# Kernel tuning notes

Measured on AMD Instinct MI355X. Metric: run time of the kernel, lower is better.

## Reference

```python
import jax, jax.numpy as jnp
import numpy as np

COV_EMB = 32
N_HEAD = 2
FACTOR_TCL = 2   # TemporalConvolutionalLayer factor (default 2)
FACTOR_MLP = 1   # MLP factor passed from MultiAttention init
EPS = 1e-5


def _conv1d_causal(x, w, b):
    # x: [N, C, T], w: [O, C, 3]; torch pads 2 both sides then slices [..., :-2],
    # equivalent to left-pad 2 only -> output length T.
    y = jax.lax.conv_general_dilated(x, w, window_strides=(1,), padding=[(2, 0)],
                                     dimension_numbers=('NCH', 'OIH', 'NCH'))
    return y + b[None, :, None]


def _tcl(x, w_conv, b_conv, w_proj, b_proj):
    # TemporalConvolutionalLayer: x [..., T, C] -> [..., T, C]
    shp = x.shape
    T, C = shp[-2], shp[-1]
    x2 = x.reshape(-1, T, C).transpose(0, 2, 1)              # [N, C, T]
    h = jax.nn.gelu(_conv1d_causal(x2, w_conv, b_conv), approximate=False)
    h = h.transpose(0, 2, 1)                                  # [N, T, 2C]
    out = h @ w_proj.T + b_proj                               # [N, T, C]
    return out.reshape(*shp[:-1], C)


def _layernorm(x, w):
    mu = jnp.mean(x, axis=-1, keepdims=True)
    var = jnp.var(x, axis=-1, keepdims=True)
    return (x - mu) * jax.lax.rsqrt(var + EPS) * w


def setup_inputs() -> dict:
    key = jax.random.key(0)
    ks = jax.random.split(key, 20)
    C = COV_EMB
    C2 = FACTOR_TCL * C
    s = 0.02
    inp = {
        'causal_decoder': jax.random.normal(ks[0], (8, 4, 1024, C), jnp.float32),
        'past_kv': jax.random.normal(ks[1], (8, 1024, C), jnp.float32),
    }
    def tcl_params(i):
        return (jax.random.normal(ks[i], (C2, C, 3), jnp.float32) * s,
                jnp.zeros((C2,), jnp.float32),
                jax.random.normal(ks[i + 1], (C, C2), jnp.float32) * s,
                jnp.zeros((C,), jnp.float32))
    inp['wq_conv'], inp['bq_conv'], inp['wq_proj'], inp['bq_proj'] = tcl_params(2)
    inp['wk_conv'], inp['bk_conv'], inp['wk_proj'], inp['bk_proj'] = tcl_params(4)
    inp['wv_conv'], inp['bv_conv'], inp['wv_proj'], inp['bv_proj'] = tcl_params(6)
    inp['w_cproj'] = jax.random.normal(ks[8], (C, C), jnp.float32) * s   # bias=False
    inp['ln_w'] = jnp.ones((C,), jnp.float32)                            # bias=False
    inp['w_fc'] = jax.random.normal(ks[9], (FACTOR_MLP * C, C), jnp.float32) * s   # bias=False
    inp['w_mlp_proj'] = jax.random.normal(ks[10], (C, FACTOR_MLP * C), jnp.float32) * s
    return inp


def reference(causal_decoder, past_kv,
              wq_conv, bq_conv, wq_proj, bq_proj,
              wk_conv, bk_conv, wk_proj, bk_proj,
              wv_conv, bv_conv, wv_proj, bv_proj,
              w_cproj, ln_w, w_fc, w_mlp_proj):
    B, F, T, C = causal_decoder.shape
    nh, hd = N_HEAD, C // N_HEAD

    q = _tcl(causal_decoder, wq_conv, bq_conv, wq_proj, bq_proj)   # [B,F,T,C]
    k = _tcl(past_kv, wk_conv, bk_conv, wk_proj, bk_proj)          # [B,S,C]
    v = _tcl(past_kv, wv_conv, bv_conv, wv_proj, bv_proj)          # [B,S,C]

    S = k.shape[1]
    q = q.reshape(B, F, T, nh, hd).transpose(0, 1, 3, 2, 4)        # [B,F,h,T,d]
    k = k.reshape(B, S, nh, hd).transpose(0, 2, 1, 3)              # [B,h,S,d]
    v = v.reshape(B, S, nh, hd).transpose(0, 2, 1, 3)              # [B,h,S,d]

    scale = 1.0 / jnp.sqrt(jnp.asarray(hd, q.dtype))
    scores = jnp.einsum('bfhtd,bhsd->bfhts', q, k) * scale          # [B,F,h,T,S]
    attn = jax.nn.softmax(scores, axis=-1)
    y = jnp.einsum('bfhts,bhsd->bfhtd', attn, v)                    # [B,F,h,T,d]
    y = y.transpose(0, 1, 3, 2, 4).reshape(B, F, T, C)

    out = causal_decoder + y @ w_cproj.T                            # resid_dropout = id (p=0)
    h = _layernorm(out, ln_w)
    mlp = jax.nn.gelu(h @ w_fc.T, approximate=False) @ w_mlp_proj.T
    out = out + mlp
    return out
```

## Files before the change

kernel.cpp:

```cpp
#include <hip/hip_runtime.h>
#include <hip/hip_bf16.h>

#define T_LEN 1024

typedef __attribute__((ext_vector_type(8))) short short8;
typedef __attribute__((ext_vector_type(4))) short short4v;
typedef __attribute__((ext_vector_type(4))) float float4v;
typedef __attribute__((ext_vector_type(2))) unsigned uint2v;
typedef __attribute__((ext_vector_type(4))) unsigned uint4v;

__device__ __forceinline__ float gelu_exact(float x) {
    return 0.5f * x * (1.0f + erff(x * 0.70710678118654752440f));
}
__device__ __forceinline__ unsigned short f2bf(float f) {
    unsigned u = __float_as_uint(f);
    u += 0x7fffu + ((u >> 16) & 1u);
    return (unsigned short)(u >> 16);
}
__device__ __forceinline__ unsigned pk2bf(float a, float b) {
    __hip_bfloat162 h = __float22bfloat162_rn(make_float2(a, b));
    unsigned u;
    __builtin_memcpy(&u, &h, 4);
    return u;
}

__device__ __forceinline__ short8 xpose_p(float4v t0, float4v t1) {
    unsigned u0 = pk2bf(t0.x, t0.y);
    unsigned u1 = pk2bf(t0.z, t0.w);
    unsigned u2 = pk2bf(t1.x, t1.y);
    unsigned u3 = pk2bf(t1.z, t1.w);
    uint2v r0 = __builtin_amdgcn_permlane32_swap(u0, u2, false, false);
    uint2v r1 = __builtin_amdgcn_permlane32_swap(u1, u3, false, false);
    uint2v r2 = __builtin_amdgcn_permlane16_swap(r0.x, r0.y, false, false);
    uint2v r3 = __builtin_amdgcn_permlane16_swap(r1.x, r1.y, false, false);
    uint4v p = { r2.x, r3.x, r2.y, r3.y };
    short8 f;
    __builtin_memcpy(&f, &p, 16);
    return f;
}

__global__ __launch_bounds__(256) void kv_tcl(
    const float* __restrict__ pkv,
    const float* __restrict__ wkc, const float* __restrict__ bkc,
    const float* __restrict__ wkp, const float* __restrict__ bkp,
    const float* __restrict__ wvc, const float* __restrict__ bvc,
    const float* __restrict__ wvp, const float* __restrict__ bvp,
    unsigned short* __restrict__ kbf, unsigned short* __restrict__ vtbf)
{
    __shared__ __align__(16) unsigned short Abuf[32 * 96];
    __shared__ __align__(16) unsigned short WbT[64 * 96];
    __shared__ __align__(16) unsigned short Hb[32 * 72];
    __shared__ __align__(16) unsigned short WpB[32 * 72];

    const int tid = threadIdx.x;
    const int gb = blockIdx.x;

    const float *wc, *bc, *wp, *bp;
    unsigned short* outb;
    int mode;
    if (gb < 256) { wc = wkc; bc = bkc; wp = wkp; bp = bkp; outb = kbf;  mode = 0; }
    else          { wc = wvc; bc = bvc; wp = wvp; bp = bvp; outb = vtbf; mode = 1; }
    const int n  = gb & 7;
    const int t0 = ((gb >> 3) & 31) * 32;

#pragma unroll
    for (int it = 0; it < 3; ++it) {
        int s = (tid + it * 256) >> 3;
        int sub = tid & 7;
        int t = s / 3, tap = s - t * 3;
        int tau = t0 + t - 2 + tap;
        float4 xv = make_float4(0.f, 0.f, 0.f, 0.f);
        if (tau >= 0) xv = *(const float4*)&pkv[((size_t)n * T_LEN + tau) * 32 + sub * 4];
        short4v pk = { (short)f2bf(xv.x), (short)f2bf(xv.y),
                       (short)f2bf(xv.z), (short)f2bf(xv.w) };
        *(short4v*)&Abuf[t * 96 + tap * 32 + sub * 4] = pk;
    }
#pragma unroll
    for (int it = 0; it < 6; ++it) {
        int i4 = tid + it * 256;
        int idx = i4 * 4;
        int o = idx / 96, r = idx - o * 96;
        float4 w4 = *(const float4*)&wc[idx];
        float we[4] = { w4.x, w4.y, w4.z, w4.w };
#pragma unroll
        for (int e = 0; e < 4; ++e) {
            int re = r + e, c = re / 3, tap = re - c * 3;
            WbT[o * 96 + tap * 32 + c] = f2bf(we[e]);
        }
    }
#pragma unroll
    for (int it = 0; it < 2; ++it) {
        int i4 = tid + it * 256;
        int idx = i4 * 4;
        int c = idx >> 6, o = idx & 63;
        float4 w4 = *(const float4*)&wp[idx];
        short4v pk = { (short)f2bf(w4.x), (short)f2bf(w4.y),
                       (short)f2bf(w4.z), (short)f2bf(w4.w) };
        *(short4v*)&WpB[c * 72 + o] = pk;
    }

    const int w = tid >> 6;
    const int ln = tid & 63;
    const int sn = ln & 15;
    const int quad = ln >> 4;

    const float bcv = bc[w * 16 + sn];
    const int tmw = w & 1, cnw = w >> 1;
    const float bpv = bp[cnw * 16 + sn];

    __syncthreads();

    short8 b0 = *(const short8*)&WbT[(w * 16 + sn) * 96 + 0  + quad * 8];
    short8 b1 = *(const short8*)&WbT[(w * 16 + sn) * 96 + 32 + quad * 8];
    short8 b2 = *(const short8*)&WbT[(w * 16 + sn) * 96 + 64 + quad * 8];
    float4v zero = { 0.f, 0.f, 0.f, 0.f };
    float4v acc[2] = { zero, zero };
#pragma unroll
    for (int tm = 0; tm < 2; ++tm) {
        const unsigned short* ar = &Abuf[(tm * 16 + sn) * 96 + quad * 8];
        short8 a0 = *(const short8*)(ar + 0);
        short8 a1 = *(const short8*)(ar + 32);
        short8 a2 = *(const short8*)(ar + 64);
        acc[tm] = __builtin_amdgcn_mfma_f32_16x16x32_bf16(a0, b0, acc[tm], 0, 0, 0);
        acc[tm] = __builtin_amdgcn_mfma_f32_16x16x32_bf16(a1, b1, acc[tm], 0, 0, 0);
        acc[tm] = __builtin_amdgcn_mfma_f32_16x16x32_bf16(a2, b2, acc[tm], 0, 0, 0);
    }
#pragma unroll
    for (int tm = 0; tm < 2; ++tm) {
        float ge[4];
        ge[0] = gelu_exact(acc[tm].x + bcv);
        ge[1] = gelu_exact(acc[tm].y + bcv);
        ge[2] = gelu_exact(acc[tm].z + bcv);
        ge[3] = gelu_exact(acc[tm].w + bcv);
#pragma unroll
        for (int i = 0; i < 4; ++i)
            Hb[(tm * 16 + quad * 4 + i) * 72 + w * 16 + sn] = f2bf(ge[i]);
    }

    __syncthreads();

    const unsigned short* hr = &Hb[(tmw * 16 + sn) * 72 + quad * 8];
    short8 pa0 = *(const short8*)(hr + 0);
    short8 pa1 = *(const short8*)(hr + 32);
    short8 pb0 = *(const short8*)&WpB[(cnw * 16 + sn) * 72 + quad * 8];
    short8 pb1 = *(const short8*)&WpB[(cnw * 16 + sn) * 72 + 32 + quad * 8];
    float4v pacc = zero;
    pacc = __builtin_amdgcn_mfma_f32_16x16x32_bf16(pa0, pb0, pacc, 0, 0, 0);
    pacc = __builtin_amdgcn_mfma_f32_16x16x32_bf16(pa1, pb1, pacc, 0, 0, 0);

    float v[4] = { pacc.x + bpv, pacc.y + bpv, pacc.z + bpv, pacc.w + bpv };
#pragma unroll
    for (int i = 0; i < 4; ++i) {
        int t = tmw * 16 + quad * 4 + i;
        int c = cnw * 16 + sn;
        if (mode == 0) {
            outb[((size_t)n * T_LEN + t0 + t) * 32 + c] = f2bf(v[i]);
        } else {
            outb[((size_t)(n * 2 + cnw) * 16 + sn) * T_LEN + t0 + t] = f2bf(v[i]);
        }
    }
}

__global__ __launch_bounds__(512) void fused_qae(
    const float* __restrict__ cd,
    const float* __restrict__ wqc, const float* __restrict__ bqc,
    const float* __restrict__ wqp, const float* __restrict__ bqp,
    const unsigned short* __restrict__ kbf,
    const unsigned short* __restrict__ vtbf,
    const float* __restrict__ wcp, const float* __restrict__ lnw,
    const float* __restrict__ wfc, const float* __restrict__ wmp,
    float* __restrict__ out)
{
    __shared__ __align__(16) char smem[43520];
    unsigned short* Abuf = (unsigned short*)(smem);
    unsigned short* WbT  = (unsigned short*)(smem + 12288);
    unsigned short* Hb   = (unsigned short*)(smem + 24576);
    unsigned short* WpB  = (unsigned short*)(smem + 33792);
    unsigned short* qs   = (unsigned short*)(smem + 38400);

    const int tid = threadIdx.x;
    const int bid = blockIdx.x;
    const int b  = bid & 7;
    const int f_ = (bid >> 3) & 3;
    const int bf = b * 4 + f_;
    const int tt = bid >> 5;
    const int t0 = tt * 64;
    const float SC = 0.36067376022224085f;

#pragma unroll
    for (int it = 0; it < 3; ++it) {
        int idx = tid + it * 512;
        int s = idx >> 3;
        int sub = idx & 7;
        int t = s / 3, tap = s - t * 3;
        int tau = t0 + t - 2 + tap;
        float4 xv = make_float4(0.f, 0.f, 0.f, 0.f);
        if (tau >= 0) xv = *(const float4*)&cd[((size_t)bf * T_LEN + tau) * 32 + sub * 4];
        short4v pk = { (short)f2bf(xv.x), (short)f2bf(xv.y),
                       (short)f2bf(xv.z), (short)f2bf(xv.w) };
        *(short4v*)&Abuf[t * 96 + tap * 32 + sub * 4] = pk;
    }
#pragma unroll
    for (int it = 0; it < 3; ++it) {
        int i4 = tid + it * 512;
        int idx = i4 * 4;
        int o = idx / 96, r = idx - o * 96;
        float4 w4 = *(const float4*)&wqc[idx];
        float we[4] = { w4.x, w4.y, w4.z, w4.w };
#pragma unroll
        for (int e = 0; e < 4; ++e) {
            int re = r + e, c = re / 3, tap = re - c * 3;
            WbT[o * 96 + tap * 32 + c] = f2bf(we[e]);
        }
    }
    {
        int idx = tid * 4;
        int c = idx >> 6, o = idx & 63;
        float4 w4 = *(const float4*)&wqp[idx];
        short4v pk = { (short)f2bf(w4.x), (short)f2bf(w4.y),
                       (short)f2bf(w4.z), (short)f2bf(w4.w) };
        *(short4v*)&WpB[c * 72 + o] = pk;
    }

    const int w = tid >> 6;
    const int ln = tid & 63;
    const int sn = ln & 15;
    const int quad = ln >> 4;
    const float4v zero = { 0.f, 0.f, 0.f, 0.f };

    __syncthreads();

    {
        const int tm = w & 3;
        const int on0 = w >> 2, on1 = on0 + 2;
        const unsigned short* ar = &Abuf[(tm * 16 + sn) * 96 + quad * 8];
        short8 a0 = *(const short8*)(ar + 0);
        short8 a1 = *(const short8*)(ar + 32);
        short8 a2 = *(const short8*)(ar + 64);
        const unsigned short* br0 = &WbT[(on0 * 16 + sn) * 96 + quad * 8];
        const unsigned short* br1 = &WbT[(on1 * 16 + sn) * 96 + quad * 8];
        float4v c0 = zero, c1 = zero;
        c0 = __builtin_amdgcn_mfma_f32_16x16x32_bf16(a0, *(const short8*)(br0 + 0),  c0, 0, 0, 0);
        c0 = __builtin_amdgcn_mfma_f32_16x16x32_bf16(a1, *(const short8*)(br0 + 32), c0, 0, 0, 0);
        c0 = __builtin_amdgcn_mfma_f32_16x16x32_bf16(a2, *(const short8*)(br0 + 64), c0, 0, 0, 0);
        c1 = __builtin_amdgcn_mfma_f32_16x16x32_bf16(a0, *(const short8*)(br1 + 0),  c1, 0, 0, 0);
        c1 = __builtin_amdgcn_mfma_f32_16x16x32_bf16(a1, *(const short8*)(br1 + 32), c1, 0, 0, 0);
        c1 = __builtin_amdgcn_mfma_f32_16x16x32_bf16(a2, *(const short8*)(br1 + 64), c1, 0, 0, 0);
        const float bc0 = bqc[on0 * 16 + sn], bc1 = bqc[on1 * 16 + sn];
        float g0[4] = { gelu_exact(c0.x + bc0), gelu_exact(c0.y + bc0),
                        gelu_exact(c0.z + bc0), gelu_exact(c0.w + bc0) };
        float g1[4] = { gelu_exact(c1.x + bc1), gelu_exact(c1.y + bc1),
                        gelu_exact(c1.z + bc1), gelu_exact(c1.w + bc1) };
#pragma unroll
        for (int i = 0; i < 4; ++i) {
            Hb[(tm * 16 + quad * 4 + i) * 72 + on0 * 16 + sn] = f2bf(g0[i]);
            Hb[(tm * 16 + quad * 4 + i) * 72 + on1 * 16 + sn] = f2bf(g1[i]);
        }
    }
    __syncthreads();

    {
        const int tm = w & 3, cn = w >> 2;
        const unsigned short* hr = &Hb[(tm * 16 + sn) * 72 + quad * 8];
        short8 pa0 = *(const short8*)(hr + 0);
        short8 pa1 = *(const short8*)(hr + 32);
        const unsigned short* wr_ = &WpB[(cn * 16 + sn) * 72 + quad * 8];
        short8 pb0 = *(const short8*)(wr_ + 0);
        short8 pb1 = *(const short8*)(wr_ + 32);
        float4v pacc = zero;
        pacc = __builtin_amdgcn_mfma_f32_16x16x32_bf16(pa0, pb0, pacc, 0, 0, 0);
        pacc = __builtin_amdgcn_mfma_f32_16x16x32_bf16(pa1, pb1, pacc, 0, 0, 0);
        const float bpv = bqp[cn * 16 + sn];
        float v[4] = { (pacc.x + bpv) * SC, (pacc.y + bpv) * SC,
                       (pacc.z + bpv) * SC, (pacc.w + bpv) * SC };
#pragma unroll
        for (int i = 0; i < 4; ++i)
            qs[(tm * 16 + quad * 4 + i) * 40 + cn * 16 + sn] = f2bf(v[i]);
    }

    {
        float* swc = (float*)(smem + 0);
        float* swf = (float*)(smem + 4608);
        float* swm = (float*)(smem + 9216);
        float* sln = (float*)(smem + 13824);
        for (int i = tid; i < 1024; i += 512) {
            int r = i >> 5, cc = i & 31;
            swc[r * 36 + cc] = wcp[i];
            swf[r * 36 + cc] = wfc[i];
            swm[r * 36 + cc] = wmp[i];
        }
        if (tid < 32) sln[tid] = lnw[tid];
    }
    __syncthreads();

    const int h = w & 1, rt = w >> 1;
    short8 aq = {0, 0, 0, 0, 0, 0, 0, 0};
    if (quad < 2)
        aq = *(const short8*)&qs[(rt * 16 + sn) * 40 + h * 16 + quad * 8];

    const unsigned short* kb = kbf + (size_t)b * T_LEN * 32 + h * 16 + quad * 8;
    const unsigned short* vb = vtbf + ((size_t)(b * 2 + h) * 16 + sn) * T_LEN + quad * 8;

    const short8 ones = { 16256, 16256, 16256, 16256,
                          16256, 16256, 16256, 16256 };
    float4v yacc = zero;
    float4v lacc = zero;

#pragma unroll 2
    for (int s0 = 0; s0 < 1024; s0 += 64) {
        short8 ka0 = {0,0,0,0,0,0,0,0}, ka1 = ka0, kc0 = ka0, kc1 = ka0;
        if (quad < 2) {
            ka0 = *(const short8*)(kb + (size_t)(s0 + sn) * 32);
            ka1 = *(const short8*)(kb + (size_t)(s0 + 16 + sn) * 32);
            kc0 = *(const short8*)(kb + (size_t)(s0 + 32 + sn) * 32);
            kc1 = *(const short8*)(kb + (size_t)(s0 + 48 + sn) * 32);
        }
        short8 bvA = *(const short8*)(vb + s0);
        short8 bvB = *(const short8*)(vb + s0 + 32);

        float4v cA0 = __builtin_amdgcn_mfma_f32_16x16x32_bf16(ka0, aq, zero, 0, 0, 0);
        float4v cA1 = __builtin_amdgcn_mfma_f32_16x16x32_bf16(ka1, aq, zero, 0, 0, 0);
        float4v cB0 = __builtin_amdgcn_mfma_f32_16x16x32_bf16(kc0, aq, zero, 0, 0, 0);
        float4v cB1 = __builtin_amdgcn_mfma_f32_16x16x32_bf16(kc1, aq, zero, 0, 0, 0);

        float4v eA0, eA1, eB0, eB1;
        eA0.x = exp2f(cA0.x); eA0.y = exp2f(cA0.y); eA0.z = exp2f(cA0.z); eA0.w = exp2f(cA0.w);
        eA1.x = exp2f(cA1.x); eA1.y = exp2f(cA1.y); eA1.z = exp2f(cA1.z); eA1.w = exp2f(cA1.w);
        eB0.x = exp2f(cB0.x); eB0.y = exp2f(cB0.y); eB0.z = exp2f(cB0.z); eB0.w = exp2f(cB0.w);
        eB1.x = exp2f(cB1.x); eB1.y = exp2f(cB1.y); eB1.z = exp2f(cB1.z); eB1.w = exp2f(cB1.w);

        short8 apA = xpose_p(eA0, eA1);
        short8 apB = xpose_p(eB0, eB1);

        yacc = __builtin_amdgcn_mfma_f32_16x16x32_bf16(bvA, apA, yacc, 0, 0, 0);
        yacc = __builtin_amdgcn_mfma_f32_16x16x32_bf16(bvB, apB, yacc, 0, 0, 0);
        lacc = __builtin_amdgcn_mfma_f32_16x16x32_bf16(ones, apA, lacc, 0, 0, 0);
        lacc = __builtin_amdgcn_mfma_f32_16x16x32_bf16(ones, apB, lacc, 0, 0, 0);
    }

    float* sy = (float*)(smem + 24576);
    {
        const float linv = 1.0f / lacc.x;
        float4v yn = { yacc.x * linv, yacc.y * linv,
                       yacc.z * linv, yacc.w * linv };
        *(float4v*)&sy[(rt * 16 + sn) * 32 + h * 16 + quad * 4] = yn;
    }
    __syncthreads();

    float* swc = (float*)(smem + 0);
    float* swf = (float*)(smem + 4608);
    float* swm = (float*)(smem + 9216);
    float* sln = (float*)(smem + 13824);
    float* shn = (float*)(smem + 13952);
    float* sgv = (float*)(smem + 16256);

    const int rl = tid >> 5, c = tid & 31;
    const float lnwc = sln[c];
#pragma unroll 1
    for (int p = 0; p < 4; ++p) {
        int r = p * 16 + rl;
        size_t row = (size_t)bf * T_LEN + t0 + r;
        float x1 = cd[row * 32 + c];
#pragma unroll
        for (int j4 = 0; j4 < 8; ++j4) {
            float4 yv = *(const float4*)&sy[r * 32 + j4 * 4];
            const float* wv = &swc[c * 36 + j4 * 4];
            x1 += wv[0] * yv.x + wv[1] * yv.y + wv[2] * yv.z + wv[3] * yv.w;
        }
        float s1 = x1, s2 = x1 * x1;
#pragma unroll
        for (int off = 16; off; off >>= 1) {
            s1 += __shfl_xor(s1, off);
            s2 += __shfl_xor(s2, off);
        }
        float mu = s1 * (1.0f / 32.0f);
        float var = s2 * (1.0f / 32.0f) - mu * mu;
        float hn = (x1 - mu) * rsqrtf(var + 1e-5f) * lnwc;
        shn[rl * 36 + c] = hn;
        float ga = 0.f;
#pragma unroll
        for (int j4 = 0; j4 < 8; ++j4) {
            float4 hv = *(const float4*)&shn[rl * 36 + j4 * 4];
            const float* wv = &swf[c * 36 + j4 * 4];
            ga += wv[0] * hv.x + wv[1] * hv.y + wv[2] * hv.z + wv[3] * hv.w;
        }
        float gv = gelu_exact(ga);
        sgv[rl * 36 + c] = gv;
        float oa = x1;
#pragma unroll
        for (int j4 = 0; j4 < 8; ++j4) {
            float4 gvv = *(const float4*)&sgv[rl * 36 + j4 * 4];
            const float* wv = &swm[c * 36 + j4 * 4];
            oa += wv[0] * gvv.x + wv[1] * gvv.y + wv[2] * gvv.z + wv[3] * gvv.w;
        }
        out[row * 32 + c] = oa;
    }
}

extern "C" void kernel_launch(void* const* d_in, const int* in_sizes, int n_in,
                              void* d_out, int out_size, void* d_ws, size_t ws_size,
                              hipStream_t stream) {
    const float* cd  = (const float*)d_in[0];
    const float* pkv = (const float*)d_in[1];
    const float* wqc = (const float*)d_in[2];
    const float* bqc = (const float*)d_in[3];
    const float* wqp = (const float*)d_in[4];
    const float* bqp = (const float*)d_in[5];
    const float* wkc = (const float*)d_in[6];
    const float* bkc = (const float*)d_in[7];
    const float* wkp = (const float*)d_in[8];
    const float* bkp = (const float*)d_in[9];
    const float* wvc = (const float*)d_in[10];
    const float* bvc = (const float*)d_in[11];
    const float* wvp = (const float*)d_in[12];
    const float* bvp = (const float*)d_in[13];
    const float* wcp = (const float*)d_in[14];
    const float* lnw = (const float*)d_in[15];
    const float* wfc = (const float*)d_in[16];
    const float* wmp = (const float*)d_in[17];

    unsigned short* kbf  = (unsigned short*)d_ws;
    unsigned short* vtbf = kbf + (size_t)8 * 1024 * 32;

    kv_tcl<<<512, 256, 0, stream>>>(pkv, wkc, bkc, wkp, bkp,
                                    wvc, bvc, wvp, bvp, kbf, vtbf);
    fused_qae<<<512, 512, 0, stream>>>(cd, wqc, bqc, wqp, bqp, kbf, vtbf,
                                       wcp, lnw, wfc, wmp, (float*)d_out);
}
```

Before: 133.9 us.

## Move Q TCL into the K/V TCL kernel and store scaled Q to global

The Q temporal-conv projection is taken out of the fused attention kernel and computed by the first kernel, which now launches 1536 blocks covering K, V and Q. Q is written to workspace as pre-scaled bf16, and the attention/epilogue kernel reads it from global memory. The attention kernel gets smaller LDS use and less prologue work, which may raise occupancy and shorten its critical path. In exchange there is an extra global round trip for Q and a larger first kernel.

```diff
diff --git a/kernel.cpp b/kernel.cpp
--- a/kernel.cpp
+++ b/kernel.cpp
@@ -39,13 +39,16 @@
     return f;
 }
 
-__global__ __launch_bounds__(256) void kv_tcl(
-    const float* __restrict__ pkv,
+__global__ __launch_bounds__(256) void tcl_all(
+    const float* __restrict__ cd, const float* __restrict__ pkv,
+    const float* __restrict__ wqc, const float* __restrict__ bqc,
+    const float* __restrict__ wqp, const float* __restrict__ bqp,
     const float* __restrict__ wkc, const float* __restrict__ bkc,
     const float* __restrict__ wkp, const float* __restrict__ bkp,
     const float* __restrict__ wvc, const float* __restrict__ bvc,
     const float* __restrict__ wvp, const float* __restrict__ bvp,
-    unsigned short* __restrict__ kbf, unsigned short* __restrict__ vtbf)
+    unsigned short* __restrict__ kbf, unsigned short* __restrict__ vtbf,
+    unsigned short* __restrict__ qsg)
 {
     __shared__ __align__(16) unsigned short Abuf[32 * 96];
     __shared__ __align__(16) unsigned short WbT[64 * 96];
@@ -54,14 +57,30 @@
 
     const int tid = threadIdx.x;
     const int gb = blockIdx.x;
+    const float SC = 0.36067376022224085f;
 
     const float *wc, *bc, *wp, *bp;
+    const float* inbase;
     unsigned short* outb;
-    int mode;
-    if (gb < 256) { wc = wkc; bc = bkc; wp = wkp; bp = bkp; outb = kbf;  mode = 0; }
-    else          { wc = wvc; bc = bvc; wp = wvp; bp = bvp; outb = vtbf; mode = 1; }
-    const int n  = gb & 7;
-    const int t0 = ((gb >> 3) & 31) * 32;
+    int mode, t0;
+    size_t orow;
+    if (gb < 256) {
+        mode = 0; int n = gb & 7; t0 = ((gb >> 3) & 31) * 32;
+        wc = wkc; bc = bkc; wp = wkp; bp = bkp;
+        inbase = pkv + (size_t)n * T_LEN * 32;
+        outb = kbf; orow = (size_t)n * T_LEN;
+    } else if (gb < 512) {
+        mode = 1; int n = gb & 7; t0 = ((gb >> 3) & 31) * 32;
+        wc = wvc; bc = bvc; wp = wvp; bp = bvp;
+        inbase = pkv + (size_t)n * T_LEN * 32;
+        outb = vtbf; orow = (size_t)n;
+    } else {
+        mode = 2; int qb = gb - 512; int bf = qb & 31; t0 = ((qb >> 5) & 31) * 32;
+        wc = wqc; bc = bqc; wp = wqp; bp = bqp;
+        inbase = cd + (size_t)bf * T_LEN * 32;
+        outb = qsg; orow = (size_t)bf * T_LEN;
+    }
+    const float scale = (mode == 2) ? SC : 1.0f;
 
 #pragma unroll
     for (int it = 0; it < 3; ++it) {
@@ -70,7 +89,7 @@
         int t = s / 3, tap = s - t * 3;
         int tau = t0 + t - 2 + tap;
         float4 xv = make_float4(0.f, 0.f, 0.f, 0.f);
-        if (tau >= 0) xv = *(const float4*)&pkv[((size_t)n * T_LEN + tau) * 32 + sub * 4];
+        if (tau >= 0) xv = *(const float4*)&inbase[(size_t)tau * 32 + sub * 4];
         short4v pk = { (short)f2bf(xv.x), (short)f2bf(xv.y),
                        (short)f2bf(xv.z), (short)f2bf(xv.w) };
         *(short4v*)&Abuf[t * 96 + tap * 32 + sub * 4] = pk;
@@ -148,35 +167,37 @@
     pacc = __builtin_amdgcn_mfma_f32_16x16x32_bf16(pa0, pb0, pacc, 0, 0, 0);
     pacc = __builtin_amdgcn_mfma_f32_16x16x32_bf16(pa1, pb1, pacc, 0, 0, 0);
 
-    float v[4] = { pacc.x + bpv, pacc.y + bpv, pacc.z + bpv, pacc.w + bpv };
+    float v[4] = { (pacc.x + bpv) * scale, (pacc.y + bpv) * scale,
+                   (pacc.z + bpv) * scale, (pacc.w + bpv) * scale };
 #pragma unroll
     for (int i = 0; i < 4; ++i) {
         int t = tmw * 16 + quad * 4 + i;
         int c = cnw * 16 + sn;
-        if (mode == 0) {
-            outb[((size_t)n * T_LEN + t0 + t) * 32 + c] = f2bf(v[i]);
+        if (mode == 1) {
+            outb[((orow * 2 + cnw) * 16 + sn) * T_LEN + t0 + t] = f2bf(v[i]);
         } else {
-            outb[((size_t)(n * 2 + cnw) * 16 + sn) * T_LEN + t0 + t] = f2bf(v[i]);
-        }
-    }
-}
-
-__global__ __launch_bounds__(512) void fused_qae(
+            outb[(orow + t0 + t) * 32 + c] = f2bf(v[i]);
+        }
+    }
+}
+
+__global__ __launch_bounds__(512) void attn_epi(
     const float* __restrict__ cd,
-    const float* __restrict__ wqc, const float* __restrict__ bqc,
-    const float* __restrict__ wqp, const float* __restrict__ bqp,
+    const unsigned short* __restrict__ qsg,
     const unsigned short* __restrict__ kbf,
     const unsigned short* __restrict__ vtbf,
     const float* __restrict__ wcp, const float* __restrict__ lnw,
     const float* __restrict__ wfc, const float* __restrict__ wmp,
     float* __restrict__ out)
 {
-    __shared__ __align__(16) char smem[43520];
-    unsigned short* Abuf = (unsigned short*)(smem);
-    unsigned short* WbT  = (unsigned short*)(smem + 12288);
-    unsigned short* Hb   = (unsigned short*)(smem + 24576);
-    unsigned short* WpB  = (unsigned short*)(smem + 33792);
-    unsigned short* qs   = (unsigned short*)(smem + 38400);
+    __shared__ __align__(16) char smem[26752];
+    float* swc = (float*)(smem + 0);
+    float* swf = (float*)(smem + 4608);
+    float* swm = (float*)(smem + 9216);
+    float* sln = (float*)(smem + 13824);
+    float* shn = (float*)(smem + 13952);
+    float* sgv = (float*)(smem + 16256);
+    float* sy  = (float*)(smem + 18560);
 
     const int tid = threadIdx.x;
     const int bid = blockIdx.x;
@@ -185,42 +206,14 @@
     const int bf = b * 4 + f_;
     const int tt = bid >> 5;
     const int t0 = tt * 64;
-    const float SC = 0.36067376022224085f;
-
-#pragma unroll
-    for (int it = 0; it < 3; ++it) {
-        int idx = tid + it * 512;
-        int s = idx >> 3;
-        int sub = idx & 7;
-        int t = s / 3, tap = s - t * 3;
-        int tau = t0 + t - 2 + tap;
-        float4 xv = make_float4(0.f, 0.f, 0.f, 0.f);
-        if (tau >= 0) xv = *(const float4*)&cd[((size_t)bf * T_LEN + tau) * 32 + sub * 4];
-        short4v pk = { (short)f2bf(xv.x), (short)f2bf(xv.y),
-                       (short)f2bf(xv.z), (short)f2bf(xv.w) };
-        *(short4v*)&Abuf[t * 96 + tap * 32 + sub * 4] = pk;
-    }
-#pragma unroll
-    for (int it = 0; it < 3; ++it) {
-        int i4 = tid + it * 512;
-        int idx = i4 * 4;
-        int o = idx / 96, r = idx - o * 96;
-        float4 w4 = *(const float4*)&wqc[idx];
-        float we[4] = { w4.x, w4.y, w4.z, w4.w };
-#pragma unroll
-        for (int e = 0; e < 4; ++e) {
-            int re = r + e, c = re / 3, tap = re - c * 3;
-            WbT[o * 96 + tap * 32 + c] = f2bf(we[e]);
-        }
-    }
-    {
-        int idx = tid * 4;
-        int c = idx >> 6, o = idx & 63;
-        float4 w4 = *(const float4*)&wqp[idx];
-        short4v pk = { (short)f2bf(w4.x), (short)f2bf(w4.y),
-                       (short)f2bf(w4.z), (short)f2bf(w4.w) };
-        *(short4v*)&WpB[c * 72 + o] = pk;
-    }
+
+    for (int i = tid; i < 1024; i += 512) {
+        int r = i >> 5, cc = i & 31;
+        swc[r * 36 + cc] = wcp[i];
+        swf[r * 36 + cc] = wfc[i];
+        swm[r * 36 + cc] = wmp[i];
+    }
+    if (tid < 32) sln[tid] = lnw[tid];
 
     const int w = tid >> 6;
     const int ln = tid & 63;
@@ -228,75 +221,11 @@
     const int quad = ln >> 4;
     const float4v zero = { 0.f, 0.f, 0.f, 0.f };
 
-    __syncthreads();
-
-    {
-        const int tm = w & 3;
-        const int on0 = w >> 2, on1 = on0 + 2;
-        const unsigned short* ar = &Abuf[(tm * 16 + sn) * 96 + quad * 8];
-        short8 a0 = *(const short8*)(ar + 0);
-        short8 a1 = *(const short8*)(ar + 32);
-        short8 a2 = *(const short8*)(ar + 64);
-        const unsigned short* br0 = &WbT[(on0 * 16 + sn) * 96 + quad * 8];
-        const unsigned short* br1 = &WbT[(on1 * 16 + sn) * 96 + quad * 8];
-        float4v c0 = zero, c1 = zero;
-        c0 = __builtin_amdgcn_mfma_f32_16x16x32_bf16(a0, *(const short8*)(br0 + 0),  c0, 0, 0, 0);
-        c0 = __builtin_amdgcn_mfma_f32_16x16x32_bf16(a1, *(const short8*)(br0 + 32), c0, 0, 0, 0);
-        c0 = __builtin_amdgcn_mfma_f32_16x16x32_bf16(a2, *(const short8*)(br0 + 64), c0, 0, 0, 0);
-        c1 = __builtin_amdgcn_mfma_f32_16x16x32_bf16(a0, *(const short8*)(br1 + 0),  c1, 0, 0, 0);
-        c1 = __builtin_amdgcn_mfma_f32_16x16x32_bf16(a1, *(const short8*)(br1 + 32), c1, 0, 0, 0);
-        c1 = __builtin_amdgcn_mfma_f32_16x16x32_bf16(a2, *(const short8*)(br1 + 64), c1, 0, 0, 0);
-        const float bc0 = bqc[on0 * 16 + sn], bc1 = bqc[on1 * 16 + sn];
-        float g0[4] = { gelu_exact(c0.x + bc0), gelu_exact(c0.y + bc0),
-                        gelu_exact(c0.z + bc0), gelu_exact(c0.w + bc0) };
-        float g1[4] = { gelu_exact(c1.x + bc1), gelu_exact(c1.y + bc1),
-                        gelu_exact(c1.z + bc1), gelu_exact(c1.w + bc1) };
-#pragma unroll
-        for (int i = 0; i < 4; ++i) {
-            Hb[(tm * 16 + quad * 4 + i) * 72 + on0 * 16 + sn] = f2bf(g0[i]);
-            Hb[(tm * 16 + quad * 4 + i) * 72 + on1 * 16 + sn] = f2bf(g1[i]);
-        }
-    }
-    __syncthreads();
-
-    {
-        const int tm = w & 3, cn = w >> 2;
-        const unsigned short* hr = &Hb[(tm * 16 + sn) * 72 + quad * 8];
-        short8 pa0 = *(const short8*)(hr + 0);
-        short8 pa1 = *(const short8*)(hr + 32);
-        const unsigned short* wr_ = &WpB[(cn * 16 + sn) * 72 + quad * 8];
-        short8 pb0 = *(const short8*)(wr_ + 0);
-        short8 pb1 = *(const short8*)(wr_ + 32);
-        float4v pacc = zero;
-        pacc = __builtin_amdgcn_mfma_f32_16x16x32_bf16(pa0, pb0, pacc, 0, 0, 0);
-        pacc = __builtin_amdgcn_mfma_f32_16x16x32_bf16(pa1, pb1, pacc, 0, 0, 0);
-        const float bpv = bqp[cn * 16 + sn];
-        float v[4] = { (pacc.x + bpv) * SC, (pacc.y + bpv) * SC,
-                       (pacc.z + bpv) * SC, (pacc.w + bpv) * SC };
-#pragma unroll
-        for (int i = 0; i < 4; ++i)
-            qs[(tm * 16 + quad * 4 + i) * 40 + cn * 16 + sn] = f2bf(v[i]);
-    }
-
-    {
-        float* swc = (float*)(smem + 0);
-        float* swf = (float*)(smem + 4608);
-        float* swm = (float*)(smem + 9216);
-        float* sln = (float*)(smem + 13824);
-        for (int i = tid; i < 1024; i += 512) {
-            int r = i >> 5, cc = i & 31;
-            swc[r * 36 + cc] = wcp[i];
-            swf[r * 36 + cc] = wfc[i];
-            swm[r * 36 + cc] = wmp[i];
-        }
-        if (tid < 32) sln[tid] = lnw[tid];
-    }
-    __syncthreads();
-
     const int h = w & 1, rt = w >> 1;
     short8 aq = {0, 0, 0, 0, 0, 0, 0, 0};
     if (quad < 2)
-        aq = *(const short8*)&qs[(rt * 16 + sn) * 40 + h * 16 + quad * 8];
+        aq = *(const short8*)&qsg[((size_t)bf * T_LEN + t0 + rt * 16 + sn) * 32
+                                  + h * 16 + quad * 8];
 
     const unsigned short* kb = kbf + (size_t)b * T_LEN * 32 + h * 16 + quad * 8;
     const unsigned short* vb = vtbf + ((size_t)(b * 2 + h) * 16 + sn) * T_LEN + quad * 8;
@@ -338,7 +267,6 @@
         lacc = __builtin_amdgcn_mfma_f32_16x16x32_bf16(ones, apB, lacc, 0, 0, 0);
     }
 
-    float* sy = (float*)(smem + 24576);
     {
         const float linv = 1.0f / lacc.x;
         float4v yn = { yacc.x * linv, yacc.y * linv,
@@ -346,13 +274,6 @@
         *(float4v*)&sy[(rt * 16 + sn) * 32 + h * 16 + quad * 4] = yn;
     }
     __syncthreads();
-
-    float* swc = (float*)(smem + 0);
-    float* swf = (float*)(smem + 4608);
-    float* swm = (float*)(smem + 9216);
-    float* sln = (float*)(smem + 13824);
-    float* shn = (float*)(smem + 13952);
-    float* sgv = (float*)(smem + 16256);
 
     const int rl = tid >> 5, c = tid & 31;
     const float lnwc = sln[c];
@@ -421,9 +342,11 @@
 
     unsigned short* kbf  = (unsigned short*)d_ws;
     unsigned short* vtbf = kbf + (size_t)8 * 1024 * 32;
-
-    kv_tcl<<<512, 256, 0, stream>>>(pkv, wkc, bkc, wkp, bkp,
-                                    wvc, bvc, wvp, bvp, kbf, vtbf);
-    fused_qae<<<512, 512, 0, stream>>>(cd, wqc, bqc, wqp, bqp, kbf, vtbf,
-                                       wcp, lnw, wfc, wmp, (float*)d_out);
-}
+    unsigned short* qsg  = vtbf + (size_t)8 * 1024 * 32;
+
+    tcl_all<<<1536, 256, 0, stream>>>(cd, pkv, wqc, bqc, wqp, bqp,
+                                      wkc, bkc, wkp, bkp, wvc, bvc, wvp, bvp,
+                                      kbf, vtbf, qsg);
+    attn_epi<<<512, 512, 0, stream>>>(cd, qsg, kbf, vtbf,
+                                      wcp, lnw, wfc, wmp, (float*)d_out);
+}
```

Result: no change. 135.4 us (+1.1%).
